# Optimization experiments

Hardware: AMD Instinct MI355X
Metric: run time of the kernel (lower is better)

## Reference

```python
import jax, jax.numpy as jnp
import numpy as np
import math

D_MODEL = 1024
N_HEADS = 16
HEAD_DIM = D_MODEL // N_HEADS
PAD_INDEX = 0
NEG_INF = -1e9  # matches torch masked_fill value


def setup_inputs() -> dict:
    key = jax.random.key(0)
    ks = jax.random.split(key, 10)
    b, s = 2, 2048
    x = jax.random.normal(ks[0], (b, s, D_MODEL), dtype=jnp.float32)
    input_ids = jax.random.randint(ks[1], (b, s), 0, 32000, dtype=jnp.int64)
    scale = 1.0 / math.sqrt(D_MODEL)
    def lin(k):
        kw, kb = jax.random.split(k)
        W = jax.random.uniform(kw, (D_MODEL, D_MODEL), jnp.float32, -scale, scale)
        bb = jax.random.uniform(kb, (D_MODEL,), jnp.float32, -scale, scale)
        return W, bb
    Wq, bq = lin(ks[2])
    Wk, bk = lin(ks[3])
    Wv, bv = lin(ks[4])
    Wo, bo = lin(ks[5])
    return {"x": x, "input_ids": input_ids,
            "Wq": Wq, "bq": bq, "Wk": Wk, "bk": bk,
            "Wv": Wv, "bv": bv, "Wo": Wo, "bo": bo}


def reference(x, input_ids, Wq, bq, Wk, bk, Wv, bv, Wo, bo):
    b, s, _ = x.shape
    # torch nn.Linear: y = x @ W.T + b
    q = (x @ Wq.T + bq).reshape(b, s, N_HEADS, HEAD_DIM)
    k = (x @ Wk.T + bk).reshape(b, s, N_HEADS, HEAD_DIM)
    v = (x @ Wv.T + bv).reshape(b, s, N_HEADS, HEAD_DIM)
    # scores: [b, h, s, s]
    scores = jnp.einsum('bqhd,bkhd->bhqk', q, k) / math.sqrt(HEAD_DIM)
    pad_mask = (input_ids != PAD_INDEX)[:, None, None, :]          # [b,1,1,s] over keys
    causal = jnp.tril(jnp.ones((s, s), dtype=bool))[None, None]     # [1,1,s,s]
    final_mask = pad_mask & causal
    scores = jnp.where(final_mask, scores, NEG_INF)
    attn = jax.nn.softmax(scores, axis=-1)
    out = jnp.einsum('bhqk,bkhd->bqhd', attn, v).reshape(b, s, D_MODEL)
    return out @ Wo.T + bo
```

## Files before the change

### kernel.cpp

```cpp
#include <hip/hip_runtime.h>

#define DMODEL 1024
#define NHEADS 16
#define HDIM   64
#define BATCH  2
#define SEQ    2048
#define MROWS  (BATCH*SEQ)

typedef __bf16 bf16x8 __attribute__((ext_vector_type(8)));
typedef float floatx4 __attribute__((ext_vector_type(4)));

typedef const __attribute__((address_space(1))) void gvoid;
typedef __attribute__((address_space(3))) void lvoid;

__device__ inline unsigned short f2bf(float f) {
  unsigned int u = __float_as_uint(f);
  u += 0x7fffu + ((u >> 16) & 1u);
  return (unsigned short)(u >> 16);
}

__global__ void cast_f32_bf16(const float* __restrict__ in,
                              unsigned short* __restrict__ out, int n4) {
  int i = blockIdx.x * blockDim.x + threadIdx.x;
  if (i < n4) {
    float4 f = ((const float4*)in)[i];
    ((ushort4*)out)[i] = make_ushort4(f2bf(f.x), f2bf(f.y), f2bf(f.z), f2bf(f.w));
  }
}

__global__ void cast_w4(const float* __restrict__ a, const float* __restrict__ b,
                        const float* __restrict__ c, const float* __restrict__ d,
                        unsigned short* __restrict__ oa, unsigned short* __restrict__ ob,
                        unsigned short* __restrict__ oc, unsigned short* __restrict__ od) {
  const int i = blockIdx.x * blockDim.x + threadIdx.x;
  const float* s = blockIdx.y == 0 ? a : blockIdx.y == 1 ? b : blockIdx.y == 2 ? c : d;
  unsigned short* o = blockIdx.y == 0 ? oa : blockIdx.y == 1 ? ob : blockIdx.y == 2 ? oc : od;
  float4 f = ((const float4*)s)[i];
  ((ushort4*)o)[i] = make_ushort4(f2bf(f.x), f2bf(f.y), f2bf(f.z), f2bf(f.w));
}

template<int MODE>
__global__ __launch_bounds__(256)
void gemm_nt(const unsigned short* __restrict__ A,
             const unsigned short* __restrict__ W0,
             const unsigned short* __restrict__ W1,
             const unsigned short* __restrict__ W2,
             const float* __restrict__ b0,
             const float* __restrict__ b1,
             const float* __restrict__ b2,
             unsigned short* __restrict__ qout,
             unsigned short* __restrict__ kout,
             unsigned short* __restrict__ vout,
             float* __restrict__ outf)
{
  const int K = DMODEL;
  __shared__ unsigned short As[128*32];
  __shared__ unsigned short Bs[128*32];
  const int tid  = threadIdx.x;
  const int wid  = tid >> 6;
  const int lane = tid & 63;
  const int brow = blockIdx.y * 128;
  const int bcol = blockIdx.x * 128;
  const int wr = (wid >> 1) * 64;
  const int wc = (wid & 1) * 64;

  int which = 0;
  const unsigned short* Bw = W0;
  const float* bias = b0;
  int bcolL = bcol;
  if (MODE == 0) {
    which = bcol >> 10;
    Bw   = which == 0 ? W0 : which == 1 ? W1 : W2;
    bias = which == 0 ? b0 : which == 1 ? b1 : b2;
    bcolL = bcol & 1023;
  }

  floatx4 acc[4][4] = {};

  const int sr = wid*16 + (lane >> 2);
  const int sc = (lane & 3) * 8;
  const int fr = lane & 15;
  const int fk = (lane >> 4) * 8;

  for (int kt = 0; kt < K; kt += 32) {
    __syncthreads();
#pragma unroll
    for (int i = 0; i < 2; ++i) {
      __builtin_amdgcn_global_load_lds(
          (gvoid*)(A + (size_t)(brow + i*64 + sr)*K + kt + sc),
          (lvoid*)(As + i*2048 + wid*512), 16, 0, 0);
      __builtin_amdgcn_global_load_lds(
          (gvoid*)(Bw + (size_t)(bcolL + i*64 + sr)*K + kt + sc),
          (lvoid*)(Bs + i*2048 + wid*512), 16, 0, 0);
    }
    __syncthreads();
    bf16x8 af[4], bfv[4];
#pragma unroll
    for (int m = 0; m < 4; ++m)
      af[m] = *(const bf16x8*)(As + (wr + m*16 + fr)*32 + fk);
#pragma unroll
    for (int n = 0; n < 4; ++n)
      bfv[n] = *(const bf16x8*)(Bs + (wc + n*16 + fr)*32 + fk);
#pragma unroll
    for (int m = 0; m < 4; ++m)
#pragma unroll
      for (int n = 0; n < 4; ++n)
        acc[m][n] = __builtin_amdgcn_mfma_f32_16x16x32_bf16(af[m], bfv[n], acc[m][n], 0, 0, 0);
  }

  const int er = (lane >> 4) * 4;
  const int ec = lane & 15;
#pragma unroll
  for (int m = 0; m < 4; ++m) {
#pragma unroll
    for (int n = 0; n < 4; ++n) {
      const int colL = bcolL + wc + n*16 + ec;
      const float bv = bias[colL];
#pragma unroll
      for (int j = 0; j < 4; ++j) {
        const int row = brow + wr + m*16 + er + j;
        const float val = acc[m][n][j] + bv;
        if (MODE == 0) {
          const int bi = row >> 11, s = row & 2047;
          const int hh = colL >> 6, dd = colL & 63;
          if (which == 2)
            vout[((size_t)(bi*NHEADS + hh)*HDIM + dd)*SEQ + s] = f2bf(val);
          else {
            unsigned short* o = (which == 0) ? qout : kout;
            o[((size_t)(bi*NHEADS + hh)*SEQ + s)*HDIM + dd] = f2bf(val);
          }
        } else {
          outf[(size_t)row*DMODEL + bcol + wc + n*16 + ec] = val;
        }
      }
    }
  }
}

__global__ __launch_bounds__(256, 2)
void attn_fwd(const unsigned short* __restrict__ qb,
              const unsigned short* __restrict__ kb,
              const unsigned short* __restrict__ vtb,
              const int* __restrict__ ids,
              unsigned short* __restrict__ outb)
{
  const int hb = blockIdx.x;
  const int pr = blockIdx.y;
  const int h = hb & 15, bi = hb >> 4;

  const int tid = threadIdx.x, wid = tid >> 6, lane = tid & 63;
  const size_t hoff = (size_t)(bi*NHEADS + h) * SEQ * HDIM;
  const unsigned short* Qh  = qb  + hoff;
  const unsigned short* Kh  = kb  + hoff;
  const unsigned short* Vth = vtb + hoff;

  __shared__ unsigned short Ks[2][128*64];
  __shared__ unsigned short Vs[2][64*128];
  __shared__ unsigned short Ps[4][16*128];

  const int q_   = lane & 15;
  const int hi4  = lane >> 4;
  const int koff = hi4 * 4;
  const float SC2 = 0.125f * 1.44269504088896f;

  const int krow0 = tid >> 3;
  const int ksw   = ((tid & 7) ^ ((tid >> 3) & 7)) * 8;
  const int vrow0 = tid >> 4;
  const int vsw   = ((tid & 15) ^ ((tid >> 4) & 7)) * 8;

#define STAGE(T, B) do {                                                       \
    const unsigned short* kbase_ = Kh + (size_t)(T)*128*HDIM;                  \
    const unsigned short* vbase_ = Vth + (size_t)(T)*128;                      \
    _Pragma("unroll")                                                          \
    for (int i_ = 0; i_ < 4; ++i_)                                             \
      __builtin_amdgcn_global_load_lds(                                        \
          (gvoid*)(kbase_ + (size_t)(krow0 + i_*32)*HDIM + ksw),               \
          (lvoid*)(Ks[B] + (tid + i_*256)*8), 16, 0, 0);                       \
    _Pragma("unroll")                                                          \
    for (int i_ = 0; i_ < 4; ++i_)                                             \
      __builtin_amdgcn_global_load_lds(                                        \
          (gvoid*)(vbase_ + (size_t)(vrow0 + i_*16)*SEQ + vsw),                \
          (lvoid*)(Vs[B] + (tid + i_*256)*8), 16, 0, 0);                       \
  } while (0)

  for (int half = 0; half < 2; ++half) {
    const int qt = half ? 31 - pr : pr;
    const int qbase = qt * 64;
    const int qg = qbase + wid*16 + q_;
    bf16x8 qf[2];
#pragma unroll
    for (int c = 0; c < 2; ++c)
      qf[c] = *(const bf16x8*)(Qh + (size_t)qg*HDIM + c*32 + hi4*8);

    float m2 = -INFINITY, l_run = 0.f;
    floatx4 Oacc[4] = {};

    const int nT = (qt >> 1) + 1;
    STAGE(0, 0);

    for (int kbv = 0; kbv < nT; ++kbv) {
      const int kb0 = kbv * 128;
      const int bufc = kbv & 1;
      const int pv0 = ids[bi*SEQ + kb0 + lane];
      const int pv1 = ids[bi*SEQ + kb0 + 64 + lane];
      if (kbv + 1 < nT) {
        STAGE(kbv + 1, bufc ^ 1);
        asm volatile("s_waitcnt vmcnt(8)" ::: "memory");
      } else {
        asm volatile("s_waitcnt vmcnt(0)" ::: "memory");
      }
      const unsigned long long wma = __ballot(pv0 == 0);
      const unsigned long long wmb = __ballot(pv1 == 0);
      __builtin_amdgcn_s_barrier();
      __builtin_amdgcn_sched_barrier(0);

      floatx4 st[8];
#pragma unroll
      for (int t = 0; t < 8; ++t) {
        st[t] = (floatx4){0.f, 0.f, 0.f, 0.f};
        const int kr = t*16 + q_;
#pragma unroll
        for (int c = 0; c < 2; ++c) {
          const int cd = ((c*4 + hi4) ^ (kr & 7)) * 8;
          bf16x8 kf = *(const bf16x8*)(Ks[bufc] + kr*64 + cd);
          st[t] = __builtin_amdgcn_mfma_f32_16x16x32_bf16(kf, qf[c], st[t], 0, 0, 0);
        }
      }

      float vals[32];
      if (((wma | wmb) == 0ull) && (kbv + 1 < nT)) {
#pragma unroll
        for (int t = 0; t < 8; ++t)
#pragma unroll
          for (int r = 0; r < 4; ++r) vals[t*4+r] = st[t][r];
      } else {
#pragma unroll
        for (int t = 0; t < 8; ++t)
#pragma unroll
          for (int r = 0; r < 4; ++r) {
            const int ko = t*16 + koff + r;
            const unsigned long long wm = (t < 4) ? wma : wmb;
            const bool dead = ((kb0 + ko) > qg) || (((wm >> (ko & 63)) & 1ull) != 0ull);
            vals[t*4+r] = dead ? -3.0e12f : st[t][r];
          }
      }

      float g[8];
#pragma unroll
      for (int t = 0; t < 8; ++t)
        g[t] = fmaxf(fmaxf(vals[t*4], vals[t*4+1]), fmaxf(vals[t*4+2], vals[t*4+3]));
      float tmax = fmaxf(fmaxf(fmaxf(g[0], g[1]), fmaxf(g[2], g[3])),
                         fmaxf(fmaxf(g[4], g[5]), fmaxf(g[6], g[7])));
      tmax = fmaxf(tmax, __shfl_xor(tmax, 16));
      tmax = fmaxf(tmax, __shfl_xor(tmax, 32));
      const float m2cand = tmax * SC2;

      if (!__all(m2cand <= m2 + 8.f)) {
        const float m2new = fmaxf(m2, m2cand);
        const float alpha = exp2f(m2 - m2new);
        l_run *= alpha;
#pragma unroll
        for (int r = 0; r < 4; ++r) {
          const float ar = __shfl(alpha, koff + r);
          Oacc[0][r] *= ar; Oacc[1][r] *= ar; Oacc[2][r] *= ar; Oacc[3][r] *= ar;
        }
        m2 = m2new;
      }

      float psum = 0.f;
      unsigned short* Pw = Ps[wid];
#pragma unroll
      for (int t = 0; t < 8; ++t) {
        const float p0 = exp2f(__builtin_fmaf(vals[t*4+0], SC2, -m2));
        const float p1 = exp2f(__builtin_fmaf(vals[t*4+1], SC2, -m2));
        const float p2 = exp2f(__builtin_fmaf(vals[t*4+2], SC2, -m2));
        const float p3 = exp2f(__builtin_fmaf(vals[t*4+3], SC2, -m2));
        psum += (p0 + p1) + (p2 + p3);
        const int cl = t*2 + (hi4 >> 1);
        *(ushort4*)(Pw + q_*128 + ((cl ^ (q_ & 7)) * 8) + ((hi4 & 1) * 4)) =
            make_ushort4(f2bf(p0), f2bf(p1), f2bf(p2), f2bf(p3));
      }
      psum += __shfl_xor(psum, 16);
      psum += __shfl_xor(psum, 32);
      l_run += psum;

#pragma unroll
      for (int ks = 0; ks < 4; ++ks) {
        const int cl = ks*4 + hi4;
        bf16x8 pf = *(const bf16x8*)(Pw + q_*128 + ((cl ^ (q_ & 7)) * 8));
#pragma unroll
        for (int n = 0; n < 4; ++n) {
          const int d = n*16 + q_;
          bf16x8 vf = *(const bf16x8*)(Vs[bufc] + d*128 + ((cl ^ (d & 7)) * 8));
          Oacc[n] = __builtin_amdgcn_mfma_f32_16x16x32_bf16(pf, vf, Oacc[n], 0, 0, 0);
        }
      }
      __builtin_amdgcn_s_barrier();
    }

#pragma unroll
    for (int r = 0; r < 4; ++r) {
      const float lr = __shfl(l_run, koff + r);
      const float inv = 1.f / lr;
      const int row = bi*SEQ + qbase + wid*16 + koff + r;
#pragma unroll
      for (int n = 0; n < 4; ++n)
        outb[(size_t)row*DMODEL + h*HDIM + n*16 + q_] = f2bf(Oacc[n][r] * inv);
    }
  }
#undef STAGE
}

extern "C" void kernel_launch(void* const* d_in, const int* in_sizes, int n_in,
                              void* d_out, int out_size, void* d_ws, size_t ws_size,
                              hipStream_t stream)
{
  const float* x  = (const float*)d_in[0];
  const int*   ids= (const int*)d_in[1];
  const float* Wq = (const float*)d_in[2];
  const float* bq = (const float*)d_in[3];
  const float* Wk = (const float*)d_in[4];
  const float* bk = (const float*)d_in[5];
  const float* Wv = (const float*)d_in[6];
  const float* bv = (const float*)d_in[7];
  const float* Wo = (const float*)d_in[8];
  const float* bo = (const float*)d_in[9];
  float* out = (float*)d_out;

  char* ws = (char*)d_ws;
  unsigned short* xb   = (unsigned short*)(ws);
  unsigned short* wqb  = (unsigned short*)(ws + ( 8u<<20));
  unsigned short* wkb  = (unsigned short*)(ws + (10u<<20));
  unsigned short* wvb  = (unsigned short*)(ws + (12u<<20));
  unsigned short* wob  = (unsigned short*)(ws + (14u<<20));
  unsigned short* qbuf = (unsigned short*)(ws + (16u<<20));
  unsigned short* kbuf = (unsigned short*)(ws + (24u<<20));
  unsigned short* vbuf = (unsigned short*)(ws + (32u<<20));
  unsigned short* abuf = (unsigned short*)(ws + (40u<<20));

  cast_f32_bf16<<<4096, 256, 0, stream>>>(x, xb, MROWS*DMODEL/4);
  cast_w4<<<dim3(1024, 4), 256, 0, stream>>>(Wq, Wk, Wv, Wo, wqb, wkb, wvb, wob);

  gemm_nt<0><<<dim3(24, 32), 256, 0, stream>>>(xb, wqb, wkb, wvb, bq, bk, bv,
                                               qbuf, kbuf, vbuf, nullptr);

  attn_fwd<<<dim3(32, 16), 256, 0, stream>>>(qbuf, kbuf, vbuf, ids, abuf);

  gemm_nt<1><<<dim3(8, 32), 256, 0, stream>>>(abuf, wob, wob, wob, bo, bo, bo,
                                              nullptr, nullptr, nullptr, out);
}
```

Measured before the change: 127.2 us.

## Merge casts, remap GEMM blocks, precompute pad masks, specialize attention tail tiles

Fuses the two cast kernels into one launch and uses hardware bf16 conversion in place of manual rounding. The GEMMs get a 1D grid remapped so consecutive blocks spread across row tiles, with vectorized V-transpose stores. The attention kernel precomputes padding bitmasks in LDS once per block and templates the tile step on tile width and masking. The diagonal tile runs a half-width step when possible, and setprio hints wrap the MFMA sections. Together these aim to cut launch overhead, redundant id loads and wasted masked work, at the cost of more code paths and extra LDS.

```diff
diff --git a/kernel.cpp b/kernel.cpp
--- a/kernel.cpp
+++ b/kernel.cpp
@@ -8,35 +8,35 @@
 #define MROWS  (BATCH*SEQ)
 
 typedef __bf16 bf16x8 __attribute__((ext_vector_type(8)));
+typedef __bf16 bf16x4 __attribute__((ext_vector_type(4)));
 typedef float floatx4 __attribute__((ext_vector_type(4)));
 
 typedef const __attribute__((address_space(1))) void gvoid;
 typedef __attribute__((address_space(3))) void lvoid;
 
-__device__ inline unsigned short f2bf(float f) {
-  unsigned int u = __float_as_uint(f);
-  u += 0x7fffu + ((u >> 16) & 1u);
-  return (unsigned short)(u >> 16);
-}
-
-__global__ void cast_f32_bf16(const float* __restrict__ in,
-                              unsigned short* __restrict__ out, int n4) {
-  int i = blockIdx.x * blockDim.x + threadIdx.x;
-  if (i < n4) {
-    float4 f = ((const float4*)in)[i];
-    ((ushort4*)out)[i] = make_ushort4(f2bf(f.x), f2bf(f.y), f2bf(f.z), f2bf(f.w));
-  }
-}
-
-__global__ void cast_w4(const float* __restrict__ a, const float* __restrict__ b,
-                        const float* __restrict__ c, const float* __restrict__ d,
-                        unsigned short* __restrict__ oa, unsigned short* __restrict__ ob,
-                        unsigned short* __restrict__ oc, unsigned short* __restrict__ od) {
-  const int i = blockIdx.x * blockDim.x + threadIdx.x;
-  const float* s = blockIdx.y == 0 ? a : blockIdx.y == 1 ? b : blockIdx.y == 2 ? c : d;
-  unsigned short* o = blockIdx.y == 0 ? oa : blockIdx.y == 1 ? ob : blockIdx.y == 2 ? oc : od;
-  float4 f = ((const float4*)s)[i];
-  ((ushort4*)o)[i] = make_ushort4(f2bf(f.x), f2bf(f.y), f2bf(f.z), f2bf(f.w));
+template<int V>  struct ICi { static constexpr int  value = V; };
+template<bool V> struct ICb { static constexpr bool value = V; };
+
+__global__ void cast_all(const float* __restrict__ x,
+                         const float* __restrict__ wq, const float* __restrict__ wk,
+                         const float* __restrict__ wv, const float* __restrict__ wo,
+                         __bf16* __restrict__ xb, __bf16* __restrict__ wqb,
+                         __bf16* __restrict__ wkb, __bf16* __restrict__ wvb,
+                         __bf16* __restrict__ wob)
+{
+  const int i = blockIdx.x * 256 + threadIdx.x;
+  const float* s; __bf16* o; int off;
+  if (i < MROWS*DMODEL/4) { s = x; o = xb; off = i; }
+  else {
+    const int r = i - MROWS*DMODEL/4;
+    const int w = r >> 18;
+    off = r & 262143;
+    s = (w == 0) ? wq : (w == 1) ? wk : (w == 2) ? wv : wo;
+    o = (w == 0) ? wqb : (w == 1) ? wkb : (w == 2) ? wvb : wob;
+  }
+  const float4 f = ((const float4*)s)[off];
+  bf16x4 v = {(__bf16)f.x, (__bf16)f.y, (__bf16)f.z, (__bf16)f.w};
+  *(bf16x4*)(o + off*4) = v;
 }
 
 template<int MODE>
@@ -59,8 +59,14 @@
   const int tid  = threadIdx.x;
   const int wid  = tid >> 6;
   const int lane = tid & 63;
-  const int brow = blockIdx.y * 128;
-  const int bcol = blockIdx.x * 128;
+
+  const int lin = blockIdx.x;
+  const int wg  = (MODE == 0) ? ((lin & 7)*96 + (lin >> 3))
+                              : ((lin & 7)*32 + (lin >> 3));
+  const int bx  = (MODE == 0) ? (wg % 24) : (wg & 7);
+  const int by  = (MODE == 0) ? (wg / 24) : (wg >> 3);
+  const int brow = by * 128;
+  const int bcol = bx * 128;
   const int wr = (wid >> 1) * 64;
   const int wc = (wid & 1) * 64;
 
@@ -116,22 +122,24 @@
     for (int n = 0; n < 4; ++n) {
       const int colL = bcolL + wc + n*16 + ec;
       const float bv = bias[colL];
-#pragma unroll
-      for (int j = 0; j < 4; ++j) {
-        const int row = brow + wr + m*16 + er + j;
-        const float val = acc[m][n][j] + bv;
-        if (MODE == 0) {
-          const int bi = row >> 11, s = row & 2047;
-          const int hh = colL >> 6, dd = colL & 63;
-          if (which == 2)
-            vout[((size_t)(bi*NHEADS + hh)*HDIM + dd)*SEQ + s] = f2bf(val);
-          else {
-            unsigned short* o = (which == 0) ? qout : kout;
-            o[((size_t)(bi*NHEADS + hh)*SEQ + s)*HDIM + dd] = f2bf(val);
-          }
+      const int rowb = brow + wr + m*16 + er;
+      if (MODE == 0) {
+        const int bi = rowb >> 11, s = rowb & 2047;
+        const int hh = colL >> 6, dd = colL & 63;
+        if (which == 2) {
+          bf16x4 v4 = {(__bf16)(acc[m][n][0] + bv), (__bf16)(acc[m][n][1] + bv),
+                       (__bf16)(acc[m][n][2] + bv), (__bf16)(acc[m][n][3] + bv)};
+          *(bf16x4*)((__bf16*)vout + ((size_t)(bi*NHEADS + hh)*HDIM + dd)*SEQ + s) = v4;
         } else {
-          outf[(size_t)row*DMODEL + bcol + wc + n*16 + ec] = val;
+          __bf16* o = (__bf16*)((which == 0) ? qout : kout);
+#pragma unroll
+          for (int j = 0; j < 4; ++j)
+            o[((size_t)(bi*NHEADS + hh)*SEQ + s + j)*HDIM + dd] = (__bf16)(acc[m][n][j] + bv);
         }
+      } else {
+#pragma unroll
+        for (int j = 0; j < 4; ++j)
+          outf[(size_t)(rowb + j)*DMODEL + colL] = acc[m][n][j] + bv;
       }
     }
   }
@@ -157,6 +165,19 @@
   __shared__ unsigned short Ks[2][128*64];
   __shared__ unsigned short Vs[2][64*128];
   __shared__ unsigned short Ps[4][16*128];
+  __shared__ unsigned int   padw[SEQ/32];
+
+#pragma unroll
+  for (int it = 0; it < SEQ/256; ++it) {
+    const int key = it*256 + tid;
+    const unsigned long long m = __ballot(ids[bi*SEQ + key] == 0);
+    if (lane == 0) {
+      const int base = (it*256 + wid*64) >> 5;
+      padw[base]   = (unsigned int)m;
+      padw[base+1] = (unsigned int)(m >> 32);
+    }
+  }
+  __syncthreads();
 
   const int q_   = lane & 15;
   const int hi4  = lane >> 4;
@@ -167,6 +188,7 @@
   const int ksw   = ((tid & 7) ^ ((tid >> 3) & 7)) * 8;
   const int vrow0 = tid >> 4;
   const int vsw   = ((tid & 15) ^ ((tid >> 4) & 7)) * 8;
+  unsigned short* Pw = Ps[wid];
 
 #define STAGE(T, B) do {                                                       \
     const unsigned short* kbase_ = Kh + (size_t)(T)*128*HDIM;                  \
@@ -195,28 +217,15 @@
     float m2 = -INFINITY, l_run = 0.f;
     floatx4 Oacc[4] = {};
 
-    const int nT = (qt >> 1) + 1;
-    STAGE(0, 0);
-
-    for (int kbv = 0; kbv < nT; ++kbv) {
-      const int kb0 = kbv * 128;
-      const int bufc = kbv & 1;
-      const int pv0 = ids[bi*SEQ + kb0 + lane];
-      const int pv1 = ids[bi*SEQ + kb0 + 64 + lane];
-      if (kbv + 1 < nT) {
-        STAGE(kbv + 1, bufc ^ 1);
-        asm volatile("s_waitcnt vmcnt(8)" ::: "memory");
-      } else {
-        asm volatile("s_waitcnt vmcnt(0)" ::: "memory");
-      }
-      const unsigned long long wma = __ballot(pv0 == 0);
-      const unsigned long long wmb = __ballot(pv1 == 0);
-      __builtin_amdgcn_s_barrier();
-      __builtin_amdgcn_sched_barrier(0);
-
-      floatx4 st[8];
-#pragma unroll
-      for (int t = 0; t < 8; ++t) {
+    auto step = [&](auto TLc, auto Mc, int kb0, int bufc,
+                    unsigned long long wma, unsigned long long wmb) {
+      constexpr int TL = decltype(TLc)::value;
+      constexpr bool MASKED = decltype(Mc)::value;
+
+      floatx4 st[TL];
+      __builtin_amdgcn_s_setprio(1);
+#pragma unroll
+      for (int t = 0; t < TL; ++t) {
         st[t] = (floatx4){0.f, 0.f, 0.f, 0.f};
         const int kr = t*16 + q_;
 #pragma unroll
@@ -226,16 +235,12 @@
           st[t] = __builtin_amdgcn_mfma_f32_16x16x32_bf16(kf, qf[c], st[t], 0, 0, 0);
         }
       }
-
-      float vals[32];
-      if (((wma | wmb) == 0ull) && (kbv + 1 < nT)) {
-#pragma unroll
-        for (int t = 0; t < 8; ++t)
-#pragma unroll
-          for (int r = 0; r < 4; ++r) vals[t*4+r] = st[t][r];
-      } else {
-#pragma unroll
-        for (int t = 0; t < 8; ++t)
+      __builtin_amdgcn_s_setprio(0);
+
+      float vals[4*TL];
+      if (MASKED) {
+#pragma unroll
+        for (int t = 0; t < TL; ++t)
 #pragma unroll
           for (int r = 0; r < 4; ++r) {
             const int ko = t*16 + koff + r;
@@ -243,14 +248,22 @@
             const bool dead = ((kb0 + ko) > qg) || (((wm >> (ko & 63)) & 1ull) != 0ull);
             vals[t*4+r] = dead ? -3.0e12f : st[t][r];
           }
-      }
-
-      float g[8];
-#pragma unroll
-      for (int t = 0; t < 8; ++t)
+      } else {
+#pragma unroll
+        for (int t = 0; t < TL; ++t)
+#pragma unroll
+          for (int r = 0; r < 4; ++r) vals[t*4+r] = st[t][r];
+      }
+
+      float g[TL];
+#pragma unroll
+      for (int t = 0; t < TL; ++t)
         g[t] = fmaxf(fmaxf(vals[t*4], vals[t*4+1]), fmaxf(vals[t*4+2], vals[t*4+3]));
-      float tmax = fmaxf(fmaxf(fmaxf(g[0], g[1]), fmaxf(g[2], g[3])),
-                         fmaxf(fmaxf(g[4], g[5]), fmaxf(g[6], g[7])));
+#pragma unroll
+      for (int sN = TL >> 1; sN; sN >>= 1)
+#pragma unroll
+        for (int i = 0; i < sN; ++i) g[i] = fmaxf(g[i], g[i+sN]);
+      float tmax = g[0];
       tmax = fmaxf(tmax, __shfl_xor(tmax, 16));
       tmax = fmaxf(tmax, __shfl_xor(tmax, 32));
       const float m2cand = tmax * SC2;
@@ -268,24 +281,24 @@
       }
 
       float psum = 0.f;
-      unsigned short* Pw = Ps[wid];
-#pragma unroll
-      for (int t = 0; t < 8; ++t) {
+#pragma unroll
+      for (int t = 0; t < TL; ++t) {
         const float p0 = exp2f(__builtin_fmaf(vals[t*4+0], SC2, -m2));
         const float p1 = exp2f(__builtin_fmaf(vals[t*4+1], SC2, -m2));
         const float p2 = exp2f(__builtin_fmaf(vals[t*4+2], SC2, -m2));
         const float p3 = exp2f(__builtin_fmaf(vals[t*4+3], SC2, -m2));
         psum += (p0 + p1) + (p2 + p3);
+        bf16x4 pk = {(__bf16)p0, (__bf16)p1, (__bf16)p2, (__bf16)p3};
         const int cl = t*2 + (hi4 >> 1);
-        *(ushort4*)(Pw + q_*128 + ((cl ^ (q_ & 7)) * 8) + ((hi4 & 1) * 4)) =
-            make_ushort4(f2bf(p0), f2bf(p1), f2bf(p2), f2bf(p3));
+        *(bf16x4*)(Pw + q_*128 + ((cl ^ (q_ & 7)) * 8) + ((hi4 & 1) * 4)) = pk;
       }
       psum += __shfl_xor(psum, 16);
       psum += __shfl_xor(psum, 32);
       l_run += psum;
 
-#pragma unroll
-      for (int ks = 0; ks < 4; ++ks) {
+      __builtin_amdgcn_s_setprio(1);
+#pragma unroll
+      for (int ks = 0; ks < TL/2; ++ks) {
         const int cl = ks*4 + hi4;
         bf16x8 pf = *(const bf16x8*)(Pw + q_*128 + ((cl ^ (q_ & 7)) * 8));
 #pragma unroll
@@ -295,6 +308,37 @@
           Oacc[n] = __builtin_amdgcn_mfma_f32_16x16x32_bf16(pf, vf, Oacc[n], 0, 0, 0);
         }
       }
+      __builtin_amdgcn_s_setprio(0);
+    };
+
+    const int nT = (qt >> 1) + 1;
+    STAGE(0, 0);
+
+    for (int kbv = 0; kbv < nT; ++kbv) {
+      const int kb0 = kbv * 128;
+      const int bufc = kbv & 1;
+      const bool last = (kbv == nT - 1);
+      if (!last) {
+        STAGE(kbv + 1, bufc ^ 1);
+        asm volatile("s_waitcnt vmcnt(8)" ::: "memory");
+      } else {
+        asm volatile("s_waitcnt vmcnt(0)" ::: "memory");
+      }
+      const int pw = kb0 >> 5;
+      const unsigned int p0 = padw[pw],   p1 = padw[pw+1];
+      const unsigned int p2 = padw[pw+2], p3 = padw[pw+3];
+      __builtin_amdgcn_s_barrier();
+      __builtin_amdgcn_sched_barrier(0);
+      const unsigned long long wma = (unsigned long long)p0 | ((unsigned long long)p1 << 32);
+      const unsigned long long wmb = (unsigned long long)p2 | ((unsigned long long)p3 << 32);
+
+      if (!last) {
+        if ((p0 | p1 | p2 | p3) == 0u) step(ICi<8>{}, ICb<false>{}, kb0, bufc, 0ull, 0ull);
+        else                           step(ICi<8>{}, ICb<true >{}, kb0, bufc, wma, wmb);
+      } else {
+        if (qt & 1) step(ICi<8>{}, ICb<true>{}, kb0, bufc, wma, wmb);
+        else        step(ICi<4>{}, ICb<true>{}, kb0, bufc, wma, wmb);
+      }
       __builtin_amdgcn_s_barrier();
     }
 
@@ -305,7 +349,7 @@
       const int row = bi*SEQ + qbase + wid*16 + koff + r;
 #pragma unroll
       for (int n = 0; n < 4; ++n)
-        outb[(size_t)row*DMODEL + h*HDIM + n*16 + q_] = f2bf(Oacc[n][r] * inv);
+        ((__bf16*)outb)[(size_t)row*DMODEL + h*HDIM + n*16 + q_] = (__bf16)(Oacc[n][r] * inv);
     }
   }
 #undef STAGE
@@ -338,14 +382,15 @@
   unsigned short* vbuf = (unsigned short*)(ws + (32u<<20));
   unsigned short* abuf = (unsigned short*)(ws + (40u<<20));
 
-  cast_f32_bf16<<<4096, 256, 0, stream>>>(x, xb, MROWS*DMODEL/4);
-  cast_w4<<<dim3(1024, 4), 256, 0, stream>>>(Wq, Wk, Wv, Wo, wqb, wkb, wvb, wob);
-
-  gemm_nt<0><<<dim3(24, 32), 256, 0, stream>>>(xb, wqb, wkb, wvb, bq, bk, bv,
-                                               qbuf, kbuf, vbuf, nullptr);
+  cast_all<<<8192, 256, 0, stream>>>(x, Wq, Wk, Wv, Wo,
+                                     (__bf16*)xb, (__bf16*)wqb, (__bf16*)wkb,
+                                     (__bf16*)wvb, (__bf16*)wob);
+
+  gemm_nt<0><<<768, 256, 0, stream>>>(xb, wqb, wkb, wvb, bq, bk, bv,
+                                      qbuf, kbuf, vbuf, nullptr);
 
   attn_fwd<<<dim3(32, 16), 256, 0, stream>>>(qbuf, kbuf, vbuf, ids, abuf);
 
-  gemm_nt<1><<<dim3(8, 32), 256, 0, stream>>>(abuf, wob, wob, wob, bo, bo, bo,
-                                              nullptr, nullptr, nullptr, out);
+  gemm_nt<1><<<256, 256, 0, stream>>>(abuf, wob, wob, wob, bo, bo, bo,
+                                      nullptr, nullptr, nullptr, out);
 }
```

Measured after the change: 145.4 us. 1.14x slower.
